# Performance work log

Hardware: AMD Instinct MI355X
Metric: run time of the kernel (lower is better)

Reference implementation:

```python
import jax, jax.numpy as jnp
import numpy as np

D, H = 64, 16
B, S = 4, 4096
PI = 3.1415  # constant used verbatim in the original code


def setup_inputs() -> dict:
    key = jax.random.key(0)
    ks = jax.random.split(key, 11)
    inp = {
        'query': jax.random.normal(ks[0], (B, S, D), dtype=jnp.float32),
        'key': jax.random.normal(ks[1], (B, S, D), dtype=jnp.float32),
        'value': jax.random.normal(ks[2], (B, S, D), dtype=jnp.float32),
        'attn_mask': jnp.zeros((1,), dtype=bool),
        # Linear weights stored as (in, out); y = x @ W + b
        'wq_w': jax.random.normal(ks[3], (D, D * H), dtype=jnp.float32) * 0.05,
        'wq_b': jnp.zeros((D * H,), dtype=jnp.float32),
        'wk_w': jax.random.normal(ks[4], (D, D * H), dtype=jnp.float32) * 0.05,
        'wk_b': jnp.zeros((D * H,), dtype=jnp.float32),
        'wv_w': jax.random.normal(ks[5], (D, D * H), dtype=jnp.float32) * 0.05,
        'wv_b': jnp.zeros((D * H,), dtype=jnp.float32),
        'dense_w': jax.random.normal(ks[6], (D * H, D), dtype=jnp.float32) * 0.05,
        'dense_b': jnp.zeros((D,), dtype=jnp.float32),
    }
    return inp


def reference(query, key, value, attn_mask, wq_w, wq_b, wk_w, wk_b, wv_w, wv_b, dense_w, dense_b):
    b, s, _ = query.shape
    # projections -> (B, S, H, D); einsum axis n = heads
    q = (query @ wq_w + wq_b).reshape(b, s, H, D)
    k = (key @ wk_w + wk_b).reshape(b, s, H, D)
    v = (value @ wv_w + wv_b).reshape(b, s, H, D)

    q = jax.nn.elu(q) + 1.0
    k = jax.nn.elu(k) + 1.0

    pos = PI * jnp.arange(s, dtype=query.dtype) / s  # (S,)
    qc_w = jnp.cos(pos)
    qs_w = jnp.sin(pos)
    kc_w = jnp.sin(pos)  # NB: original uses sin for k_cos too (faithful)
    ks_w = jnp.sin(pos)

    q_cos = q * qc_w[None, :, None, None]
    q_sin = q * qs_w[None, :, None, None]
    k_cos = k * kc_w[None, :, None, None]
    k_sin = k * ks_w[None, :, None, None]

    def lin_attn(qf, kf):
        kv = jnp.einsum('bsnx,bsnz->bnxz', kf, v)      # (B,H,D,D)
        return jnp.einsum('bsnx,bnxz->bsnz', qf, kv)   # (B,S,H,D)

    qkv = lin_attn(q, k)
    qkv_cos = lin_attn(q_cos, k_cos)
    qkv_sin = lin_attn(q_sin, k_sin)

    denom = 1.0 / (
        jnp.einsum('bsnd,bnd->bsn', q, k.sum(axis=1))
        + jnp.einsum('bsnd,bnd->bsn', q_cos, k_cos.sum(axis=1))
        + jnp.einsum('bsnd,bnd->bsn', q_sin, k_sin.sum(axis=1))
        + 1e-05
    )

    O = (qkv + qkv_cos + qkv_sin) * denom[..., None]   # (B,S,H,D)
    concat = O.reshape(b, s, H * D)
    return concat @ dense_w + dense_b
```

## Files before the change

### kernel.cpp

```cpp
#include <hip/hip_runtime.h>
#include <math.h>

#define BB 4
#define SS 4096
#define DD 64
#define HH 16
#define PI_C 3.1415f


typedef __attribute__((ext_vector_type(8))) short short8;
typedef __attribute__((ext_vector_type(4))) float f32x4;

#define MFMA(a, b, c) __builtin_amdgcn_mfma_f32_16x16x32_bf16(a, b, c, 0, 0, 0)

__device__ __forceinline__ short f2bf(float f) {
    union { float f; unsigned u; } v; v.f = f;
    unsigned r = v.u + 0x7FFFu + ((v.u >> 16) & 1u);
    return (short)(r >> 16);
}
__device__ __forceinline__ float bf2f(short s) {
    union { unsigned u; float f; } v;
    v.u = ((unsigned)(unsigned short)s) << 16;
    return v.f;
}
__device__ __forceinline__ short8 cvt8(float4 a, float4 b) {
    short8 r;
    r[0] = f2bf(a.x); r[1] = f2bf(a.y); r[2] = f2bf(a.z); r[3] = f2bf(a.w);
    r[4] = f2bf(b.x); r[5] = f2bf(b.y); r[6] = f2bf(b.z); r[7] = f2bf(b.w);
    return r;
}
__device__ __forceinline__ float elu1(float x) { return x > 0.f ? x + 1.f : __expf(x); }
__device__ __forceinline__ void st4(short* p, short a, short b, short c, short d) {
    union { uint2 u; short s[4]; } x;
    x.s[0] = a; x.s[1] = b; x.s[2] = c; x.s[3] = d;
    *reinterpret_cast<uint2*>(p) = x.u;
}

__global__ __launch_bounds__(256, 2) void k_phase1y(
    const float* __restrict__ key, const float* __restrict__ value,
    const float* __restrict__ wk_b, const float* __restrict__ wv_b,
    const float* __restrict__ wk_w, const float* __restrict__ wv_w,
    const float* __restrict__ wq_w, const float* __restrict__ wd_w,
    float* __restrict__ pkv, float* __restrict__ pkvs,
    float* __restrict__ pks,
    short* __restrict__ wT)
{
    const int blk = blockIdx.x, t = threadIdx.x;

    __shared__ short kT[2][64 * 72], vT[2][64 * 72], vsT[2][64 * 72];
    __shared__ float ssin[512];
    __shared__ float sbk[64], sbv[64];
    __shared__ float sred[512];

    if (blk >= 512) {
        const int pb = blk - 512;
        const int h = pb & 15;
        const bool isQ = (pb < 16);
        const float* src = isQ ? wq_w : wd_w;
        const int rs = isQ ? 1024 : 64;
        const size_t srcbase = isQ ? (size_t)(h * 64) : (size_t)(h * 4096);
        short* dm = wT + (isQ ? (size_t)0 : (size_t)3 * 65536) + (size_t)h * 4096;
#pragma unroll
        for (int j = 0; j < 4; ++j) {
            int idx = j * 1024 + t * 4;
            int r = idx >> 6, c = idx & 63;
            float4 v = *reinterpret_cast<const float4*>(src + (size_t)r * rs + srcbase + c);
            dm[(c + 0) * 64 + r] = f2bf(v.x);
            dm[(c + 1) * 64 + r] = f2bf(v.y);
            dm[(c + 2) * 64 + r] = f2bf(v.z);
            dm[(c + 3) * 64 + r] = f2bf(v.w);
        }
        return;
    }

    const int chunk = blk & 7, h = (blk >> 3) & 15, b = blk >> 7;
    const int w = t >> 6, l = t & 63;
    const int lane15 = l & 15, q8 = (l >> 4) * 8, q4 = (l >> 4) * 4;

    float4 kf0, kf1, kf2, kf3, vf0, vf1, vf2, vf3;
    {
        const size_t g = ((size_t)b * SS + chunk * 512 + w * 16 + lane15) * 64 + q8;
        kf0 = *reinterpret_cast<const float4*>(key + g);
        kf1 = *reinterpret_cast<const float4*>(key + g + 4);
        kf2 = *reinterpret_cast<const float4*>(key + g + 32);
        kf3 = *reinterpret_cast<const float4*>(key + g + 36);
        vf0 = *reinterpret_cast<const float4*>(value + g);
        vf1 = *reinterpret_cast<const float4*>(value + g + 4);
        vf2 = *reinterpret_cast<const float4*>(value + g + 32);
        vf3 = *reinterpret_cast<const float4*>(value + g + 36);
    }

    short* wkL = &kT[0][0];
    short* wvL = &kT[1][0];
    {
        const int r = t >> 2, c0 = (t & 3) * 16;
        const float* pkw = wk_w + (size_t)r * 1024 + h * 64 + c0;
        const float* pvw = wv_w + (size_t)r * 1024 + h * 64 + c0;
#pragma unroll
        for (int q = 0; q < 4; ++q) {
            float4 a = *reinterpret_cast<const float4*>(pkw + q * 4);
            float4 v = *reinterpret_cast<const float4*>(pvw + q * 4);
            wkL[(c0 + q * 4 + 0) * 72 + r] = f2bf(a.x);
            wkL[(c0 + q * 4 + 1) * 72 + r] = f2bf(a.y);
            wkL[(c0 + q * 4 + 2) * 72 + r] = f2bf(a.z);
            wkL[(c0 + q * 4 + 3) * 72 + r] = f2bf(a.w);
            wvL[(c0 + q * 4 + 0) * 72 + r] = f2bf(v.x);
            wvL[(c0 + q * 4 + 1) * 72 + r] = f2bf(v.y);
            wvL[(c0 + q * 4 + 2) * 72 + r] = f2bf(v.z);
            wvL[(c0 + q * 4 + 3) * 72 + r] = f2bf(v.w);
        }
    }
    ssin[t]       = __sinf(PI_C * (float)(chunk * 512 + t)       * (1.f / 4096.f));
    ssin[t + 256] = __sinf(PI_C * (float)(chunk * 512 + t + 256) * (1.f / 4096.f));
    if (t < 64) sbk[t] = wk_b[h * 64 + t];
    else if (t < 128) sbv[t - 64] = wv_b[h * 64 + (t - 64)];
    __syncthreads();

    short8 bkf[2][4], bvf[2][4];
#pragma unroll
    for (int kss = 0; kss < 2; ++kss)
#pragma unroll
        for (int nt = 0; nt < 4; ++nt) {
            bkf[kss][nt] = *reinterpret_cast<const short8*>(&wkL[(nt * 16 + lane15) * 72 + kss * 32 + q8]);
            bvf[kss][nt] = *reinterpret_cast<const short8*>(&wvL[(nt * 16 + lane15) * 72 + kss * 32 + q8]);
        }
    __syncthreads();

    f32x4 ckv[4], ckvs[4];
#pragma unroll
    for (int i = 0; i < 4; ++i) {
        ckv[i]  = (f32x4){0.f, 0.f, 0.f, 0.f};
        ckvs[i] = (f32x4){0.f, 0.f, 0.f, 0.f};
    }
    float aks = 0.f, akss = 0.f;

    auto proj_store = [&](int buf, int sbase) {
        f32x4 ckp[4], cvp[4];
#pragma unroll
        for (int i = 0; i < 4; ++i) {
            ckp[i] = (f32x4){0.f, 0.f, 0.f, 0.f};
            cvp[i] = (f32x4){0.f, 0.f, 0.f, 0.f};
        }
        short8 ak0 = cvt8(kf0, kf1), ak1 = cvt8(kf2, kf3);
        short8 av0 = cvt8(vf0, vf1), av1 = cvt8(vf2, vf3);
#pragma unroll
        for (int nt = 0; nt < 4; ++nt) {
            ckp[nt] = MFMA(ak0, bkf[0][nt], ckp[nt]);
            cvp[nt] = MFMA(av0, bvf[0][nt], cvp[nt]);
            ckp[nt] = MFMA(ak1, bkf[1][nt], ckp[nt]);
            cvp[nt] = MFMA(av1, bvf[1][nt], cvp[nt]);
        }
        const int srel = w * 16 + q4;
#pragma unroll
        for (int nt = 0; nt < 4; ++nt) {
            const int x = nt * 16 + lane15;
            const float bk = sbk[x], bv = sbv[x];
            short ek[4], ev[4], es[4];
#pragma unroll
            for (int r = 0; r < 4; ++r) {
                float kk = elu1(ckp[nt][r] + bk);
                float vv = cvp[nt][r] + bv;
                ek[r] = f2bf(kk);
                ev[r] = f2bf(vv);
                es[r] = f2bf(vv * ssin[sbase + srel + r]);
            }
            st4(&kT [buf][x * 72 + srel], ek[0], ek[1], ek[2], ek[3]);
            st4(&vT [buf][x * 72 + srel], ev[0], ev[1], ev[2], ev[3]);
            st4(&vsT[buf][x * 72 + srel], es[0], es[1], es[2], es[3]);
        }
    };

    proj_store(0, 0);
    __syncthreads();

#pragma unroll 1
    for (int it = 0; it < 8; ++it) {
        const int cur = it & 1;
        if (it < 7) {
            const size_t g = ((size_t)b * SS + chunk * 512 + (it + 1) * 64 + w * 16 + lane15) * 64 + q8;
            kf0 = *reinterpret_cast<const float4*>(key + g);
            kf1 = *reinterpret_cast<const float4*>(key + g + 4);
            kf2 = *reinterpret_cast<const float4*>(key + g + 32);
            kf3 = *reinterpret_cast<const float4*>(key + g + 36);
            vf0 = *reinterpret_cast<const float4*>(value + g);
            vf1 = *reinterpret_cast<const float4*>(value + g + 4);
            vf2 = *reinterpret_cast<const float4*>(value + g + 32);
            vf3 = *reinterpret_cast<const float4*>(value + g + 36);
        }
#pragma unroll
        for (int kstep = 0; kstep < 2; ++kstep) {
            const int so = kstep * 32;
            short8 aV  = *reinterpret_cast<const short8*>(&vT [cur][(w * 16 + lane15) * 72 + so + q8]);
            short8 aVS = *reinterpret_cast<const short8*>(&vsT[cur][(w * 16 + lane15) * 72 + so + q8]);
#pragma unroll
            for (int nt = 0; nt < 4; ++nt) {
                short8 bK = *reinterpret_cast<const short8*>(&kT[cur][(nt * 16 + lane15) * 72 + so + q8]);
                ckv[nt]  = MFMA(aV,  bK, ckv[nt]);
                ckvs[nt] = MFMA(aVS, bK, ckvs[nt]);
            }
        }
        {
            const int sbase = it * 64;
            short8 k0 = *reinterpret_cast<const short8*>(&kT[cur][l * 72 + w * 16]);
            short8 k1 = *reinterpret_cast<const short8*>(&kT[cur][l * 72 + w * 16 + 8]);
#pragma unroll
            for (int e = 0; e < 8; ++e) {
                float fa = bf2f(k0[e]), fb = bf2f(k1[e]);
                aks  += fa + fb;
                akss += fa * ssin[sbase + w * 16 + e] + fb * ssin[sbase + w * 16 + 8 + e];
            }
        }
        if (it < 7) proj_store(cur ^ 1, (it + 1) * 64);
        __syncthreads();
    }

    const int bh = b * HH + h;
    const size_t pbase = ((size_t)(chunk * 64) + bh) * 4096;
#pragma unroll
    for (int nt = 0; nt < 4; ++nt) {
        const int x = nt * 16 + lane15;
#pragma unroll
        for (int r = 0; r < 4; ++r) {
            const int z = w * 16 + q4 + r;
            pkv [pbase + z * 64 + x] = ckv[nt][r];
            pkvs[pbase + z * 64 + x] = ckvs[nt][r];
        }
    }
    sred[t] = aks; sred[256 + t] = akss;
    __syncthreads();
    if (t < 64) {
        pks[((size_t)(chunk * 64) + bh) * 128 + t] =
            sred[t] + sred[64 + t] + sred[128 + t] + sred[192 + t];
    } else if (t < 128) {
        int tt = t - 64;
        pks[((size_t)(chunk * 64) + bh) * 128 + t] =
            sred[256 + tt] + sred[320 + tt] + sred[384 + tt] + sred[448 + tt];
    }
}

__global__ __launch_bounds__(256) void k_reduce(
    const float* __restrict__ pkv, const float* __restrict__ pkvs,
    const float* __restrict__ pks,
    short* __restrict__ kvb, short* __restrict__ kvsb,
    float* __restrict__ ksums)
{
    const int blk = blockIdx.x, t = threadIdx.x;
    if (blk < 512) {
        const float* src = (blk < 256) ? pkv : pkvs;
        short* dst = (blk < 256) ? kvb : kvsb;
        const int o4 = (blk & 255) * 256 + t;
        float4 s = make_float4(0.f, 0.f, 0.f, 0.f);
#pragma unroll
        for (int c = 0; c < 8; ++c) {
            float4 v = reinterpret_cast<const float4*>(src + (size_t)c * 262144)[o4];
            s.x += v.x; s.y += v.y; s.z += v.z; s.w += v.w;
        }
        st4(dst + (size_t)o4 * 4, f2bf(s.x), f2bf(s.y), f2bf(s.z), f2bf(s.w));
    } else {
        const int g = (blk - 512) * 256 + t;
        float4 s = make_float4(0.f, 0.f, 0.f, 0.f);
#pragma unroll
        for (int c = 0; c < 8; ++c) {
            float4 v = reinterpret_cast<const float4*>(pks + (size_t)c * 8192)[g];
            s.x += v.x; s.y += v.y; s.z += v.z; s.w += v.w;
        }
        reinterpret_cast<float4*>(ksums)[g] = s;
    }
}

__global__ __launch_bounds__(256, 2) void k_phase2(
    const float* __restrict__ query, const float* __restrict__ wq_b,
    const short* __restrict__ wqTb,
    const short* __restrict__ kvb, const short* __restrict__ kvsb,
    const float* __restrict__ ksums,
    const short* __restrict__ wdTb, const float* __restrict__ dense_b,
    float* __restrict__ out)
{
    const int st = blockIdx.x, b = blockIdx.y;
    const int s0 = st * 32;
    const int t = threadIdx.x, w = t >> 6, l = t & 63;
    const int lane15 = l & 15, q8 = (l >> 4) * 8, q4 = (l >> 4) * 4;

    __shared__ __align__(16) char smem[34816];
    __shared__ float scc[32];
    __shared__ __align__(16) float sks[2048];
    short* sqin = reinterpret_cast<short*>(smem);
    short* sqp  = reinterpret_cast<short*>(smem) + 2304 * (1 + w);
    short* sOw  = reinterpret_cast<short*>(smem) + 2304 * 5 + 1152 * w;

    {
        const int row = t >> 3, c8 = (t & 7) * 8;
        const float* qp = query + ((size_t)b * SS + s0 + row) * 64 + c8;
        float4 f0 = *reinterpret_cast<const float4*>(qp);
        float4 f1 = *reinterpret_cast<const float4*>(qp + 4);
        *reinterpret_cast<short8*>(&sqin[row * 72 + c8]) = cvt8(f0, f1);
    }
    {
        const float* kb = ksums + (size_t)b * HH * 128;
#pragma unroll
        for (int j = 0; j < 2; ++j) {
            const int o4 = j * 256 + t;
            reinterpret_cast<float4*>(sks)[o4] =
                reinterpret_cast<const float4*>(kb)[o4];
        }
    }
    if (t < 32) {
        float p = PI_C * (float)(s0 + t) * (1.f / 4096.f);
        scc[t] = __cosf(p) + __sinf(p);
    }
    f32x4 cd[2][4];
#pragma unroll
    for (int rt = 0; rt < 2; ++rt)
#pragma unroll
        for (int nt = 0; nt < 4; ++nt) cd[rt][nt] = (f32x4){0.f, 0.f, 0.f, 0.f};
    __syncthreads();

    short8 aq[2][2];
#pragma unroll
    for (int rt = 0; rt < 2; ++rt)
#pragma unroll
        for (int kss = 0; kss < 2; ++kss)
            aq[rt][kss] = *reinterpret_cast<const short8*>(&sqin[(rt * 16 + lane15) * 72 + kss * 32 + q8]);
    const float ccs0 = scc[lane15], ccs1 = scc[16 + lane15];
    const int drow = l >> 1, dxh = (l & 1) * 32;
    const float ccr = scc[drow];

#pragma unroll 1
    for (int i = 0; i < 4; ++i) {
        const int h = (i << 2) | w;
        const size_t bh = (size_t)(b * HH + h);
        const short* wqh = wqTb + (size_t)h * 4096;
        const short* wdh = wdTb + (size_t)h * 4096;
        const short* kv1 = kvb  + bh * 4096;
        const short* kv2 = kvsb + bh * 4096;

        short8 kf10[4], kf11[4], kf20[4], kf21[4];
        short8 wdf0[4], wdf1[4];
#pragma unroll
        for (int nt = 0; nt < 4; ++nt) {
            const short* a1 = kv1 + (nt * 16 + lane15) * 64;
            const short* a2 = kv2 + (nt * 16 + lane15) * 64;
            kf10[nt] = *reinterpret_cast<const short8*>(a1 + q8);
            kf11[nt] = *reinterpret_cast<const short8*>(a1 + 32 + q8);
            kf20[nt] = *reinterpret_cast<const short8*>(a2 + q8);
            kf21[nt] = *reinterpret_cast<const short8*>(a2 + 32 + q8);
            wdf0[nt] = *reinterpret_cast<const short8*>(wdh + (nt * 16 + lane15) * 64 + q8);
            wdf1[nt] = *reinterpret_cast<const short8*>(wdh + (nt * 16 + lane15) * 64 + 32 + q8);
        }

        f32x4 cq[2][4];
#pragma unroll
        for (int rt = 0; rt < 2; ++rt)
#pragma unroll
            for (int nt = 0; nt < 4; ++nt) cq[rt][nt] = (f32x4){0.f, 0.f, 0.f, 0.f};
#pragma unroll
        for (int nt = 0; nt < 4; ++nt) {
            short8 b0 = *reinterpret_cast<const short8*>(wqh + (nt * 16 + lane15) * 64 + q8);
            short8 b1 = *reinterpret_cast<const short8*>(wqh + (nt * 16 + lane15) * 64 + 32 + q8);
            cq[0][nt] = MFMA(b0, aq[0][0], cq[0][nt]);
            cq[1][nt] = MFMA(b0, aq[1][0], cq[1][nt]);
            cq[0][nt] = MFMA(b1, aq[0][1], cq[0][nt]);
            cq[1][nt] = MFMA(b1, aq[1][1], cq[1][nt]);
        }
#pragma unroll
        for (int nt = 0; nt < 4; ++nt) {
            float4 bq = *reinterpret_cast<const float4*>(wq_b + h * 64 + nt * 16 + q4);
#pragma unroll
            for (int rt = 0; rt < 2; ++rt) {
                short e0 = f2bf(elu1(cq[rt][nt][0] + bq.x));
                short e1 = f2bf(elu1(cq[rt][nt][1] + bq.y));
                short e2 = f2bf(elu1(cq[rt][nt][2] + bq.z));
                short e3 = f2bf(elu1(cq[rt][nt][3] + bq.w));
                st4(&sqp[(rt * 16 + lane15) * 72 + nt * 16 + q4], e0, e1, e2, e3);
            }
        }

        float invs0, invs1;
        {
            const float* kp = sks + h * 128 + dxh;
            float4 A[8], Bv[8];
#pragma unroll
            for (int j = 0; j < 8; ++j) {
                A[j]  = *reinterpret_cast<const float4*>(kp + j * 4);
                Bv[j] = *reinterpret_cast<const float4*>(kp + 64 + j * 4);
            }
            short8 qr[4];
#pragma unroll
            for (int e = 0; e < 4; ++e)
                qr[e] = *reinterpret_cast<const short8*>(&sqp[drow * 72 + dxh + e * 8]);
            float dsum = 0.f;
#pragma unroll
            for (int j4 = 0; j4 < 8; ++j4)
#pragma unroll
                for (int e4 = 0; e4 < 4; ++e4)
                    dsum += bf2f(qr[j4 >> 1][(j4 & 1) * 4 + e4]) * (A[j4][e4] + ccr * Bv[j4][e4]);
            dsum += __shfl_xor(dsum, 1);
            float invd = 1.f / (dsum + 1e-5f);
            invs0 = __shfl(invd, lane15 * 2);
            invs1 = __shfl(invd, (16 + lane15) * 2);
        }

        short8 qf[2][2];
#pragma unroll
        for (int rt = 0; rt < 2; ++rt)
#pragma unroll
            for (int kss = 0; kss < 2; ++kss)
                qf[rt][kss] = *reinterpret_cast<const short8*>(&sqp[(rt * 16 + lane15) * 72 + kss * 32 + q8]);
        f32x4 cv1[2][4], cv2[2][4];
#pragma unroll
        for (int rt = 0; rt < 2; ++rt)
#pragma unroll
            for (int nt = 0; nt < 4; ++nt) {
                cv1[rt][nt] = (f32x4){0.f, 0.f, 0.f, 0.f};
                cv2[rt][nt] = (f32x4){0.f, 0.f, 0.f, 0.f};
            }
#pragma unroll
        for (int nt = 0; nt < 4; ++nt) {
#pragma unroll
            for (int rt = 0; rt < 2; ++rt) {
                cv1[rt][nt] = MFMA(kf10[nt], qf[rt][0], cv1[rt][nt]);
                cv1[rt][nt] = MFMA(kf11[nt], qf[rt][1], cv1[rt][nt]);
                cv2[rt][nt] = MFMA(kf20[nt], qf[rt][0], cv2[rt][nt]);
                cv2[rt][nt] = MFMA(kf21[nt], qf[rt][1], cv2[rt][nt]);
            }
        }

#pragma unroll
        for (int rt = 0; rt < 2; ++rt) {
            const float ccsr = rt ? ccs1 : ccs0;
            const float invr = rt ? invs1 : invs0;
#pragma unroll
            for (int nt = 0; nt < 4; ++nt) {
                short e0 = f2bf((cv1[rt][nt][0] + ccsr * cv2[rt][nt][0]) * invr);
                short e1 = f2bf((cv1[rt][nt][1] + ccsr * cv2[rt][nt][1]) * invr);
                short e2 = f2bf((cv1[rt][nt][2] + ccsr * cv2[rt][nt][2]) * invr);
                short e3 = f2bf((cv1[rt][nt][3] + ccsr * cv2[rt][nt][3]) * invr);
                st4(&sOw[lane15 * 72 + nt * 16 + q4], e0, e1, e2, e3);
            }
            short8 of0 = *reinterpret_cast<const short8*>(&sOw[lane15 * 72 + q8]);
            short8 of1 = *reinterpret_cast<const short8*>(&sOw[lane15 * 72 + 32 + q8]);
#pragma unroll
            for (int nt = 0; nt < 4; ++nt) {
                cd[rt][nt] = MFMA(of0, wdf0[nt], cd[rt][nt]);
                cd[rt][nt] = MFMA(of1, wdf1[nt], cd[rt][nt]);
            }
        }
    }

    __syncthreads();
    {
        float* red = reinterpret_cast<float*>(smem) + 2176 * w;
#pragma unroll
        for (int rt = 0; rt < 2; ++rt)
#pragma unroll
            for (int nt = 0; nt < 4; ++nt)
#pragma unroll
                for (int r = 0; r < 4; ++r)
                    red[(rt * 16 + q4 + r) * 68 + nt * 16 + lane15] = cd[rt][nt][r];
    }
    __syncthreads();
    {
        const int row = t >> 3, c8 = (t & 7) * 8;
        float4 sa = make_float4(0.f, 0.f, 0.f, 0.f);
        float4 sb = make_float4(0.f, 0.f, 0.f, 0.f);
#pragma unroll
        for (int ww = 0; ww < 4; ++ww) {
            const float* red = reinterpret_cast<const float*>(smem) + 2176 * ww;
            float4 v0 = *reinterpret_cast<const float4*>(red + row * 68 + c8);
            float4 v1 = *reinterpret_cast<const float4*>(red + row * 68 + c8 + 4);
            sa.x += v0.x; sa.y += v0.y; sa.z += v0.z; sa.w += v0.w;
            sb.x += v1.x; sb.y += v1.y; sb.z += v1.z; sb.w += v1.w;
        }
        float4 d0 = *reinterpret_cast<const float4*>(dense_b + c8);
        float4 d1 = *reinterpret_cast<const float4*>(dense_b + c8 + 4);
        sa.x += d0.x; sa.y += d0.y; sa.z += d0.z; sa.w += d0.w;
        sb.x += d1.x; sb.y += d1.y; sb.z += d1.z; sb.w += d1.w;
        float* op = out + ((size_t)b * SS + s0 + row) * 64 + c8;
        *reinterpret_cast<float4*>(op)     = sa;
        *reinterpret_cast<float4*>(op + 4) = sb;
    }
}

extern "C" void kernel_launch(void* const* d_in, const int* in_sizes, int n_in,
                              void* d_out, int out_size, void* d_ws, size_t ws_size,
                              hipStream_t stream) {
    const float* query   = (const float*)d_in[0];
    const float* key     = (const float*)d_in[1];
    const float* value   = (const float*)d_in[2];
    const float* wq_w    = (const float*)d_in[4];
    const float* wq_b    = (const float*)d_in[5];
    const float* wk_w    = (const float*)d_in[6];
    const float* wk_b    = (const float*)d_in[7];
    const float* wv_w    = (const float*)d_in[8];
    const float* wv_b    = (const float*)d_in[9];
    const float* dense_w = (const float*)d_in[10];
    const float* dense_b = (const float*)d_in[11];
    float* out = (float*)d_out;

    char* ws = (char*)d_ws;
    float* pkv   = (float*)(ws);
    float* pkvs  = (float*)(ws + 8388608);
    float* pks   = (float*)(ws + 16777216);
    short* kvb   = (short*)(ws + 17039360);
    short* kvsb  = (short*)(ws + 17563648);
    float* ksums = (float*)(ws + 18087936);
    short* wT    = (short*)(ws + 18120704);
    short* wqTb  = wT;
    short* wdTb  = wT + 196608;

    hipLaunchKernelGGL(k_phase1y, dim3(544), dim3(256), 0, stream,
                       key, value, wk_b, wv_b, wk_w, wv_w, wq_w, dense_w,
                       pkv, pkvs, pks, wT);
    hipLaunchKernelGGL(k_reduce, dim3(520), dim3(256), 0, stream,
                       pkv, pkvs, pks, kvb, kvsb, ksums);
    hipLaunchKernelGGL(k_phase2, dim3(128, BB), dim3(256), 0, stream,
                       query, wq_b, wqTb, kvb, kvsb, ksums, wdTb, dense_b, out);
}
```

Baseline: 144.0 us.

## Enlarge phase2 tiles to 64 rows with 8 waves each handling two heads

k_phase2 now runs 512-thread blocks over 64 sequence rows. Each of the 8 waves handles 2 heads over two 32-row halves, where before 4 waves each handled 4 heads on 32 rows. The kv fragments loaded per head are reused across both row halves, and the dense-weight fragments are now reloaded inside the inner loop instead of held in registers. The output reduction across waves is done in two passes through shared memory, with more syncs. This halves the block count to 256 and raises shared memory and register pressure per block, which may cut occupancy.

```diff
diff --git a/kernel.cpp b/kernel.cpp
--- a/kernel.cpp
+++ b/kernel.cpp
@@ -268,7 +268,7 @@
     }
 }
 
-__global__ __launch_bounds__(256, 2) void k_phase2(
+__global__ __launch_bounds__(512, 2) void k_phase2(
     const float* __restrict__ query, const float* __restrict__ wq_b,
     const short* __restrict__ wqTb,
     const short* __restrict__ kvb, const short* __restrict__ kvsb,
@@ -277,16 +277,15 @@
     float* __restrict__ out)
 {
     const int st = blockIdx.x, b = blockIdx.y;
-    const int s0 = st * 32;
+    const int s0 = st * 64;
     const int t = threadIdx.x, w = t >> 6, l = t & 63;
     const int lane15 = l & 15, q8 = (l >> 4) * 8, q4 = (l >> 4) * 4;
 
-    __shared__ __align__(16) char smem[34816];
-    __shared__ float scc[32];
+    __shared__ __align__(16) char smem[46080];
+    __shared__ float scc[64];
     __shared__ __align__(16) float sks[2048];
     short* sqin = reinterpret_cast<short*>(smem);
-    short* sqp  = reinterpret_cast<short*>(smem) + 2304 * (1 + w);
-    short* sOw  = reinterpret_cast<short*>(smem) + 2304 * 5 + 1152 * w;
+    short* sqp  = reinterpret_cast<short*>(smem) + 4608 + 2304 * w;
 
     {
         const int row = t >> 3, c8 = (t & 7) * 8;
@@ -297,37 +296,26 @@
     }
     {
         const float* kb = ksums + (size_t)b * HH * 128;
-#pragma unroll
-        for (int j = 0; j < 2; ++j) {
-            const int o4 = j * 256 + t;
-            reinterpret_cast<float4*>(sks)[o4] =
-                reinterpret_cast<const float4*>(kb)[o4];
-        }
-    }
-    if (t < 32) {
+        reinterpret_cast<float4*>(sks)[t] = reinterpret_cast<const float4*>(kb)[t];
+    }
+    if (t < 64) {
         float p = PI_C * (float)(s0 + t) * (1.f / 4096.f);
         scc[t] = __cosf(p) + __sinf(p);
     }
-    f32x4 cd[2][4];
-#pragma unroll
-    for (int rt = 0; rt < 2; ++rt)
-#pragma unroll
-        for (int nt = 0; nt < 4; ++nt) cd[rt][nt] = (f32x4){0.f, 0.f, 0.f, 0.f};
+    f32x4 cd[2][2][4];
+#pragma unroll
+    for (int hf = 0; hf < 2; ++hf)
+#pragma unroll
+        for (int rt = 0; rt < 2; ++rt)
+#pragma unroll
+            for (int nt = 0; nt < 4; ++nt) cd[hf][rt][nt] = (f32x4){0.f, 0.f, 0.f, 0.f};
     __syncthreads();
 
-    short8 aq[2][2];
-#pragma unroll
-    for (int rt = 0; rt < 2; ++rt)
-#pragma unroll
-        for (int kss = 0; kss < 2; ++kss)
-            aq[rt][kss] = *reinterpret_cast<const short8*>(&sqin[(rt * 16 + lane15) * 72 + kss * 32 + q8]);
-    const float ccs0 = scc[lane15], ccs1 = scc[16 + lane15];
     const int drow = l >> 1, dxh = (l & 1) * 32;
-    const float ccr = scc[drow];
 
 #pragma unroll 1
-    for (int i = 0; i < 4; ++i) {
-        const int h = (i << 2) | w;
+    for (int hi = 0; hi < 2; ++hi) {
+        const int h = hi * 8 + w;
         const size_t bh = (size_t)(b * HH + h);
         const short* wqh = wqTb + (size_t)h * 4096;
         const short* wdh = wdTb + (size_t)h * 4096;
@@ -335,7 +323,6 @@
         const short* kv2 = kvsb + bh * 4096;
 
         short8 kf10[4], kf11[4], kf20[4], kf21[4];
-        short8 wdf0[4], wdf1[4];
 #pragma unroll
         for (int nt = 0; nt < 4; ++nt) {
             const short* a1 = kv1 + (nt * 16 + lane15) * 64;
@@ -344,140 +331,162 @@
             kf11[nt] = *reinterpret_cast<const short8*>(a1 + 32 + q8);
             kf20[nt] = *reinterpret_cast<const short8*>(a2 + q8);
             kf21[nt] = *reinterpret_cast<const short8*>(a2 + 32 + q8);
-            wdf0[nt] = *reinterpret_cast<const short8*>(wdh + (nt * 16 + lane15) * 64 + q8);
-            wdf1[nt] = *reinterpret_cast<const short8*>(wdh + (nt * 16 + lane15) * 64 + 32 + q8);
-        }
-
-        f32x4 cq[2][4];
-#pragma unroll
-        for (int rt = 0; rt < 2; ++rt)
-#pragma unroll
-            for (int nt = 0; nt < 4; ++nt) cq[rt][nt] = (f32x4){0.f, 0.f, 0.f, 0.f};
-#pragma unroll
-        for (int nt = 0; nt < 4; ++nt) {
-            short8 b0 = *reinterpret_cast<const short8*>(wqh + (nt * 16 + lane15) * 64 + q8);
-            short8 b1 = *reinterpret_cast<const short8*>(wqh + (nt * 16 + lane15) * 64 + 32 + q8);
-            cq[0][nt] = MFMA(b0, aq[0][0], cq[0][nt]);
-            cq[1][nt] = MFMA(b0, aq[1][0], cq[1][nt]);
-            cq[0][nt] = MFMA(b1, aq[0][1], cq[0][nt]);
-            cq[1][nt] = MFMA(b1, aq[1][1], cq[1][nt]);
-        }
-#pragma unroll
-        for (int nt = 0; nt < 4; ++nt) {
-            float4 bq = *reinterpret_cast<const float4*>(wq_b + h * 64 + nt * 16 + q4);
+        }
+
+#pragma unroll
+        for (int hf = 0; hf < 2; ++hf) {
+            const int rbase = hf * 32;
+
+            short8 aq0[2], aq1[2];
 #pragma unroll
             for (int rt = 0; rt < 2; ++rt) {
-                short e0 = f2bf(elu1(cq[rt][nt][0] + bq.x));
-                short e1 = f2bf(elu1(cq[rt][nt][1] + bq.y));
-                short e2 = f2bf(elu1(cq[rt][nt][2] + bq.z));
-                short e3 = f2bf(elu1(cq[rt][nt][3] + bq.w));
-                st4(&sqp[(rt * 16 + lane15) * 72 + nt * 16 + q4], e0, e1, e2, e3);
-            }
-        }
-
-        float invs0, invs1;
+                aq0[rt] = *reinterpret_cast<const short8*>(&sqin[(rbase + rt * 16 + lane15) * 72 + q8]);
+                aq1[rt] = *reinterpret_cast<const short8*>(&sqin[(rbase + rt * 16 + lane15) * 72 + 32 + q8]);
+            }
+            f32x4 cq[2][4];
+#pragma unroll
+            for (int rt = 0; rt < 2; ++rt)
+#pragma unroll
+                for (int nt = 0; nt < 4; ++nt) cq[rt][nt] = (f32x4){0.f, 0.f, 0.f, 0.f};
+#pragma unroll
+            for (int nt = 0; nt < 4; ++nt) {
+                short8 b0 = *reinterpret_cast<const short8*>(wqh + (nt * 16 + lane15) * 64 + q8);
+                short8 b1 = *reinterpret_cast<const short8*>(wqh + (nt * 16 + lane15) * 64 + 32 + q8);
+                cq[0][nt] = MFMA(b0, aq0[0], cq[0][nt]);
+                cq[1][nt] = MFMA(b0, aq0[1], cq[1][nt]);
+                cq[0][nt] = MFMA(b1, aq1[0], cq[0][nt]);
+                cq[1][nt] = MFMA(b1, aq1[1], cq[1][nt]);
+            }
+#pragma unroll
+            for (int nt = 0; nt < 4; ++nt) {
+                float4 bq = *reinterpret_cast<const float4*>(wq_b + h * 64 + nt * 16 + q4);
+#pragma unroll
+                for (int rt = 0; rt < 2; ++rt) {
+                    short e0 = f2bf(elu1(cq[rt][nt][0] + bq.x));
+                    short e1 = f2bf(elu1(cq[rt][nt][1] + bq.y));
+                    short e2 = f2bf(elu1(cq[rt][nt][2] + bq.z));
+                    short e3 = f2bf(elu1(cq[rt][nt][3] + bq.w));
+                    st4(&sqp[(rt * 16 + lane15) * 72 + nt * 16 + q4], e0, e1, e2, e3);
+                }
+            }
+
+            float invs0, invs1;
+            {
+                const float ccr = scc[rbase + drow];
+                const float* kp = sks + h * 128 + dxh;
+                float4 A[8], Bv[8];
+#pragma unroll
+                for (int j = 0; j < 8; ++j) {
+                    A[j]  = *reinterpret_cast<const float4*>(kp + j * 4);
+                    Bv[j] = *reinterpret_cast<const float4*>(kp + 64 + j * 4);
+                }
+                short8 qr[4];
+#pragma unroll
+                for (int e = 0; e < 4; ++e)
+                    qr[e] = *reinterpret_cast<const short8*>(&sqp[drow * 72 + dxh + e * 8]);
+                float dsum = 0.f;
+#pragma unroll
+                for (int j4 = 0; j4 < 8; ++j4)
+#pragma unroll
+                    for (int e4 = 0; e4 < 4; ++e4)
+                        dsum += bf2f(qr[j4 >> 1][(j4 & 1) * 4 + e4]) * (A[j4][e4] + ccr * Bv[j4][e4]);
+                dsum += __shfl_xor(dsum, 1);
+                float invd = 1.f / (dsum + 1e-5f);
+                invs0 = __shfl(invd, lane15 * 2);
+                invs1 = __shfl(invd, (16 + lane15) * 2);
+            }
+
+            short8 qf[2][2];
+#pragma unroll
+            for (int rt = 0; rt < 2; ++rt)
+#pragma unroll
+                for (int kss = 0; kss < 2; ++kss)
+                    qf[rt][kss] = *reinterpret_cast<const short8*>(&sqp[(rt * 16 + lane15) * 72 + kss * 32 + q8]);
+            f32x4 cv1[2][4], cv2[2][4];
+#pragma unroll
+            for (int rt = 0; rt < 2; ++rt)
+#pragma unroll
+                for (int nt = 0; nt < 4; ++nt) {
+                    cv1[rt][nt] = (f32x4){0.f, 0.f, 0.f, 0.f};
+                    cv2[rt][nt] = (f32x4){0.f, 0.f, 0.f, 0.f};
+                }
+#pragma unroll
+            for (int nt = 0; nt < 4; ++nt) {
+#pragma unroll
+                for (int rt = 0; rt < 2; ++rt) {
+                    cv1[rt][nt] = MFMA(kf10[nt], qf[rt][0], cv1[rt][nt]);
+                    cv1[rt][nt] = MFMA(kf11[nt], qf[rt][1], cv1[rt][nt]);
+                    cv2[rt][nt] = MFMA(kf20[nt], qf[rt][0], cv2[rt][nt]);
+                    cv2[rt][nt] = MFMA(kf21[nt], qf[rt][1], cv2[rt][nt]);
+                }
+            }
+
+            const float ccs0 = scc[rbase + lane15], ccs1 = scc[rbase + 16 + lane15];
+#pragma unroll
+            for (int rt = 0; rt < 2; ++rt) {
+                const float ccsr = rt ? ccs1 : ccs0;
+                const float invr = rt ? invs1 : invs0;
+#pragma unroll
+                for (int nt = 0; nt < 4; ++nt) {
+                    short e0 = f2bf((cv1[rt][nt][0] + ccsr * cv2[rt][nt][0]) * invr);
+                    short e1 = f2bf((cv1[rt][nt][1] + ccsr * cv2[rt][nt][1]) * invr);
+                    short e2 = f2bf((cv1[rt][nt][2] + ccsr * cv2[rt][nt][2]) * invr);
+                    short e3 = f2bf((cv1[rt][nt][3] + ccsr * cv2[rt][nt][3]) * invr);
+                    st4(&sqp[(rt * 16 + lane15) * 72 + nt * 16 + q4], e0, e1, e2, e3);
+                }
+                short8 of0 = *reinterpret_cast<const short8*>(&sqp[(rt * 16 + lane15) * 72 + q8]);
+                short8 of1 = *reinterpret_cast<const short8*>(&sqp[(rt * 16 + lane15) * 72 + 32 + q8]);
+#pragma unroll
+                for (int nt = 0; nt < 4; ++nt) {
+                    short8 wd0 = *reinterpret_cast<const short8*>(wdh + (nt * 16 + lane15) * 64 + q8);
+                    short8 wd1 = *reinterpret_cast<const short8*>(wdh + (nt * 16 + lane15) * 64 + 32 + q8);
+                    cd[hf][rt][nt] = MFMA(of0, wd0, cd[hf][rt][nt]);
+                    cd[hf][rt][nt] = MFMA(of1, wd1, cd[hf][rt][nt]);
+                }
+            }
+        }
+    }
+
+#pragma unroll 1
+    for (int hf = 0; hf < 2; ++hf) {
+        __syncthreads();
+        float* red = reinterpret_cast<float*>(smem) + 2176 * (w & 3);
+        if (w < 4) {
+#pragma unroll
+            for (int rt = 0; rt < 2; ++rt)
+#pragma unroll
+                for (int nt = 0; nt < 4; ++nt)
+#pragma unroll
+                    for (int r = 0; r < 4; ++r)
+                        red[(rt * 16 + q4 + r) * 68 + nt * 16 + lane15] =
+                            (hf == 0) ? cd[0][rt][nt][r] : cd[1][rt][nt][r];
+        }
+        __syncthreads();
+        if (w >= 4) {
+#pragma unroll
+            for (int rt = 0; rt < 2; ++rt)
+#pragma unroll
+                for (int nt = 0; nt < 4; ++nt)
+#pragma unroll
+                    for (int r = 0; r < 4; ++r)
+                        red[(rt * 16 + q4 + r) * 68 + nt * 16 + lane15] +=
+                            (hf == 0) ? cd[0][rt][nt][r] : cd[1][rt][nt][r];
+        }
+        __syncthreads();
         {
-            const float* kp = sks + h * 128 + dxh;
-            float4 A[8], Bv[8];
-#pragma unroll
-            for (int j = 0; j < 8; ++j) {
-                A[j]  = *reinterpret_cast<const float4*>(kp + j * 4);
-                Bv[j] = *reinterpret_cast<const float4*>(kp + 64 + j * 4);
-            }
-            short8 qr[4];
-#pragma unroll
-            for (int e = 0; e < 4; ++e)
-                qr[e] = *reinterpret_cast<const short8*>(&sqp[drow * 72 + dxh + e * 8]);
-            float dsum = 0.f;
-#pragma unroll
-            for (int j4 = 0; j4 < 8; ++j4)
-#pragma unroll
-                for (int e4 = 0; e4 < 4; ++e4)
-                    dsum += bf2f(qr[j4 >> 1][(j4 & 1) * 4 + e4]) * (A[j4][e4] + ccr * Bv[j4][e4]);
-            dsum += __shfl_xor(dsum, 1);
-            float invd = 1.f / (dsum + 1e-5f);
-            invs0 = __shfl(invd, lane15 * 2);
-            invs1 = __shfl(invd, (16 + lane15) * 2);
-        }
-
-        short8 qf[2][2];
-#pragma unroll
-        for (int rt = 0; rt < 2; ++rt)
-#pragma unroll
-            for (int kss = 0; kss < 2; ++kss)
-                qf[rt][kss] = *reinterpret_cast<const short8*>(&sqp[(rt * 16 + lane15) * 72 + kss * 32 + q8]);
-        f32x4 cv1[2][4], cv2[2][4];
-#pragma unroll
-        for (int rt = 0; rt < 2; ++rt)
-#pragma unroll
-            for (int nt = 0; nt < 4; ++nt) {
-                cv1[rt][nt] = (f32x4){0.f, 0.f, 0.f, 0.f};
-                cv2[rt][nt] = (f32x4){0.f, 0.f, 0.f, 0.f};
-            }
-#pragma unroll
-        for (int nt = 0; nt < 4; ++nt) {
-#pragma unroll
-            for (int rt = 0; rt < 2; ++rt) {
-                cv1[rt][nt] = MFMA(kf10[nt], qf[rt][0], cv1[rt][nt]);
-                cv1[rt][nt] = MFMA(kf11[nt], qf[rt][1], cv1[rt][nt]);
-                cv2[rt][nt] = MFMA(kf20[nt], qf[rt][0], cv2[rt][nt]);
-                cv2[rt][nt] = MFMA(kf21[nt], qf[rt][1], cv2[rt][nt]);
-            }
-        }
-
-#pragma unroll
-        for (int rt = 0; rt < 2; ++rt) {
-            const float ccsr = rt ? ccs1 : ccs0;
-            const float invr = rt ? invs1 : invs0;
-#pragma unroll
-            for (int nt = 0; nt < 4; ++nt) {
-                short e0 = f2bf((cv1[rt][nt][0] + ccsr * cv2[rt][nt][0]) * invr);
-                short e1 = f2bf((cv1[rt][nt][1] + ccsr * cv2[rt][nt][1]) * invr);
-                short e2 = f2bf((cv1[rt][nt][2] + ccsr * cv2[rt][nt][2]) * invr);
-                short e3 = f2bf((cv1[rt][nt][3] + ccsr * cv2[rt][nt][3]) * invr);
-                st4(&sOw[lane15 * 72 + nt * 16 + q4], e0, e1, e2, e3);
-            }
-            short8 of0 = *reinterpret_cast<const short8*>(&sOw[lane15 * 72 + q8]);
-            short8 of1 = *reinterpret_cast<const short8*>(&sOw[lane15 * 72 + 32 + q8]);
-#pragma unroll
-            for (int nt = 0; nt < 4; ++nt) {
-                cd[rt][nt] = MFMA(of0, wdf0[nt], cd[rt][nt]);
-                cd[rt][nt] = MFMA(of1, wdf1[nt], cd[rt][nt]);
-            }
-        }
-    }
-
-    __syncthreads();
-    {
-        float* red = reinterpret_cast<float*>(smem) + 2176 * w;
-#pragma unroll
-        for (int rt = 0; rt < 2; ++rt)
-#pragma unroll
-            for (int nt = 0; nt < 4; ++nt)
-#pragma unroll
-                for (int r = 0; r < 4; ++r)
-                    red[(rt * 16 + q4 + r) * 68 + nt * 16 + lane15] = cd[rt][nt][r];
-    }
-    __syncthreads();
-    {
-        const int row = t >> 3, c8 = (t & 7) * 8;
-        float4 sa = make_float4(0.f, 0.f, 0.f, 0.f);
-        float4 sb = make_float4(0.f, 0.f, 0.f, 0.f);
-#pragma unroll
-        for (int ww = 0; ww < 4; ++ww) {
-            const float* red = reinterpret_cast<const float*>(smem) + 2176 * ww;
-            float4 v0 = *reinterpret_cast<const float4*>(red + row * 68 + c8);
-            float4 v1 = *reinterpret_cast<const float4*>(red + row * 68 + c8 + 4);
-            sa.x += v0.x; sa.y += v0.y; sa.z += v0.z; sa.w += v0.w;
-            sb.x += v1.x; sb.y += v1.y; sb.z += v1.z; sb.w += v1.w;
-        }
-        float4 d0 = *reinterpret_cast<const float4*>(dense_b + c8);
-        float4 d1 = *reinterpret_cast<const float4*>(dense_b + c8 + 4);
-        sa.x += d0.x; sa.y += d0.y; sa.z += d0.z; sa.w += d0.w;
-        sb.x += d1.x; sb.y += d1.y; sb.z += d1.z; sb.w += d1.w;
-        float* op = out + ((size_t)b * SS + s0 + row) * 64 + c8;
-        *reinterpret_cast<float4*>(op)     = sa;
-        *reinterpret_cast<float4*>(op + 4) = sb;
+            const int row = t >> 4, c4 = (t & 15) * 4;
+            float4 s = make_float4(0.f, 0.f, 0.f, 0.f);
+#pragma unroll
+            for (int ww = 0; ww < 4; ++ww) {
+                const float* rb = reinterpret_cast<const float*>(smem) + 2176 * ww;
+                float4 v = *reinterpret_cast<const float4*>(rb + row * 68 + c4);
+                s.x += v.x; s.y += v.y; s.z += v.z; s.w += v.w;
+            }
+            float4 db = *reinterpret_cast<const float4*>(dense_b + c4);
+            s.x += db.x; s.y += db.y; s.z += db.z; s.w += db.w;
+            *reinterpret_cast<float4*>(
+                out + ((size_t)b * SS + s0 + hf * 32 + row) * 64 + c4) = s;
+        }
     }
 }
 
@@ -513,6 +522,6 @@
                        pkv, pkvs, pks, wT);
     hipLaunchKernelGGL(k_reduce, dim3(520), dim3(256), 0, stream,
                        pkv, pkvs, pks, kvb, kvsb, ksums);
-    hipLaunchKernelGGL(k_phase2, dim3(128, BB), dim3(256), 0, stream,
+    hipLaunchKernelGGL(k_phase2, dim3(64, BB), dim3(512), 0, stream,
                        query, wq_b, wqTb, kvb, kvsb, ksums, wdTb, dense_b, out);
 }
```

Measured after the change: 139.8 us, median of 2. 2.9% less time.
